# Kernel tuning notes

Hardware: AMD Instinct MI355X
Metric: run time of the kernel (lower is better)

Reference implementation:

```python
import jax, jax.numpy as jnp
import numpy as np

N_NODES = 50000
N_EDGES = 600000
IN_DIM = 128
LATENT = 128
OUT_DIM = 40
NUM_LAYERS = 2


def setup_inputs() -> dict:
    key = jax.random.key(0)
    ks = jax.random.split(key, 8)
    nodes_feats = jax.random.normal(ks[0], (N_NODES, IN_DIM), dtype=jnp.float32)
    adj_list = jax.random.randint(ks[1], (N_EDGES, 2), 0, N_NODES, dtype=jnp.int64)
    s_in = 1.0 / np.sqrt(IN_DIM)
    s_cb = 1.0 / np.sqrt(2 * LATENT)
    s_out = 1.0 / np.sqrt(LATENT)
    W_in = jax.random.uniform(ks[2], (IN_DIM, LATENT), jnp.float32, -s_in, s_in)
    b_in = jnp.zeros((LATENT,), jnp.float32)
    W_comb = jax.random.uniform(ks[3], (NUM_LAYERS, 2 * LATENT, LATENT), jnp.float32, -s_cb, s_cb)
    b_comb = jnp.zeros((NUM_LAYERS, LATENT), jnp.float32)
    W_out = jax.random.uniform(ks[4], (LATENT, OUT_DIM), jnp.float32, -s_out, s_out)
    b_out = jnp.zeros((OUT_DIM,), jnp.float32)
    return {"nodes_feats": nodes_feats, "adj_list": adj_list, "W_in": W_in, "b_in": b_in,
            "W_comb": W_comb, "b_comb": b_comb, "W_out": W_out, "b_out": b_out}


def reference(nodes_feats, adj_list, W_in, b_in, W_comb, b_comb, W_out, b_out):
    n = nodes_feats.shape[0]
    fro = adj_list[:, 0]
    to = adj_list[:, 1]
    # initialize: project input features to latent space
    h = jax.nn.relu(nodes_feats @ W_in + b_in)  # [N, LATENT]
    # in-degree for mean aggregation (replaces per-node Python stack+mean)
    deg = jax.ops.segment_sum(jnp.ones(fro.shape[0], h.dtype), to, num_segments=n)
    inv_deg = 1.0 / jnp.maximum(deg, 1.0)  # guard isolated nodes
    for l in range(W_comb.shape[0]):
        # gather neighbor feats along edges, scatter-add to destinations, mean
        msg = jax.ops.segment_sum(h[fro], to, num_segments=n) * inv_deg[:, None]
        # combine: ReLU(Linear([node || message]))
        h = jax.nn.relu(jnp.concatenate([h, msg], axis=-1) @ W_comb[l] + b_comb[l])
    # output head (logits for CrossEntropyLoss)
    return h @ W_out + b_out
```

## Files before the change

kernel.cpp:

```cpp
#include <hip/hip_runtime.h>
#include <hip/hip_fp16.h>

#define N_NODES 50000
#define N_EDGES 600000
#define NBLK 49

typedef unsigned int u32;
typedef _Float16 v8h __attribute__((ext_vector_type(8)));
typedef _Float16 v4h __attribute__((ext_vector_type(4)));
typedef float v4f __attribute__((ext_vector_type(4)));

__device__ __forceinline__ float2 h2f2(u32 u) {
    __half2 h = *(__half2*)&u;
    return __half22float2(h);
}

__device__ __forceinline__ int calc_mode(const int* __restrict__ adj_w) {
    int l = threadIdx.x & 63;
    unsigned long long b = __ballot(adj_w[2 * l + 1] != 0);
    return (b == 0ull) ? 1 : 0;
}
__device__ __forceinline__ int adj_to(const int* a, int m, int e) {
    return m ? a[4 * e + 2] : a[2 * e + 1];
}
__device__ __forceinline__ int adj_fro(const int* a, int m, int e) {
    return m ? a[4 * e] : a[2 * e];
}

#define COUNT_B 2344
#define WPREP_B 344
#define IN_B    1563

__global__ void k_count_prep(const int* __restrict__ adj_w, int* __restrict__ deg,
                             const float* __restrict__ W_in,
                             const float* __restrict__ W_comb,
                             const float* __restrict__ W_out,
                             _Float16* __restrict__ WinT,
                             _Float16* __restrict__ WcombT,
                             _Float16* __restrict__ WoutT) {
    if (blockIdx.x < COUNT_B) {
        int m = calc_mode(adj_w);
        int e = blockIdx.x * 256 + threadIdx.x;
        if (e < N_EDGES) atomicAdd(&deg[adj_to(adj_w, m, e)], 1);
        return;
    }
    int idx = (blockIdx.x - COUNT_B) * 256 + threadIdx.x;
    if (idx < 16384) {
        int n = idx & 127, k = idx >> 7;
        WinT[n * 128 + k] = (_Float16)W_in[k * 128 + n];
    } else if (idx < 16384 + 65536) {
        int j = idx - 16384;
        int l = j >> 15, r = j & 32767;
        int n = r & 127, k = r >> 7;
        WcombT[l * 32768 + n * 256 + k] = (_Float16)W_comb[l * 32768 + k * 128 + n];
    } else if (idx < 16384 + 65536 + 6144) {
        int j = idx - 81920;
        int n = j >> 7, k = j & 127;
        WoutT[n * 128 + k] = (n < 40) ? (_Float16)W_out[k * 40 + n] : (_Float16)0.f;
    }
}

__global__ void k_scan1(const int* __restrict__ deg, int* __restrict__ row_ptr,
                        int* __restrict__ bsum) {
    __shared__ int s[1024];
    int tid = threadIdx.x, i = blockIdx.x * 1024 + tid;
    int v = (i < N_NODES) ? deg[i] : 0;
    s[tid] = v;
    __syncthreads();
    for (int off = 1; off < 1024; off <<= 1) {
        int t = (tid >= off) ? s[tid - off] : 0;
        __syncthreads();
        s[tid] += t;
        __syncthreads();
    }
    if (i < N_NODES) row_ptr[i] = s[tid] - v;
    if (tid == 1023) bsum[blockIdx.x] = s[1023];
}

__global__ void k_scan23(const int* __restrict__ deg, int* __restrict__ row_ptr,
                         const int* __restrict__ bsum, int* __restrict__ cursor,
                         float* __restrict__ inv_deg) {
    __shared__ int sbase;
    int tid = threadIdx.x;
    if (tid < 64) {
        int v = (tid < NBLK && tid < (int)blockIdx.x) ? bsum[tid] : 0;
#pragma unroll
        for (int off = 32; off > 0; off >>= 1) v += __shfl_down(v, off);
        if (tid == 0) sbase = v;
    }
    __syncthreads();
    int i = blockIdx.x * 1024 + tid;
    if (i < N_NODES) {
        int rp = row_ptr[i] + sbase;
        row_ptr[i] = rp;
        cursor[i] = rp;
        inv_deg[i] = 1.0f / fmaxf((float)deg[i], 1.0f);
    }
    if (i == 0) row_ptr[N_NODES] = N_EDGES;
}

__global__ __launch_bounds__(256, 2) void k_fill_in(const int* __restrict__ adj_w,
                                                    int* __restrict__ cursor,
                                                    int* __restrict__ edge_src,
                                                    const float* __restrict__ X,
                                                    const _Float16* __restrict__ WT,
                                                    const float* __restrict__ bias,
                                                    _Float16* __restrict__ h) {
    __shared__ __align__(16) _Float16 xs[32][136];
    if (blockIdx.x < COUNT_B) {
        int m = calc_mode(adj_w);
        int e = blockIdx.x * 256 + threadIdx.x;
        if (e < N_EDGES) {
            int to = adj_to(adj_w, m, e);
            int slot = atomicAdd(&cursor[to], 1);
            edge_src[slot] = adj_fro(adj_w, m, e);
        }
        return;
    }
    const int t0 = threadIdx.x, w = t0 >> 6, l = t0 & 63;
    const int R0 = (blockIdx.x - COUNT_B) * 32;
    const float4* X4 = (const float4*)X;
#pragma unroll
    for (int i = 0; i < 4; i++) {
        int idx = i * 256 + t0;
        int row = idx >> 5, c4 = idx & 31;
        int rr = R0 + row;
        if (rr > N_NODES - 1) rr = N_NODES - 1;
        float4 v = X4[(size_t)rr * 32 + c4];
        v4h hv = {(_Float16)v.x, (_Float16)v.y, (_Float16)v.z, (_Float16)v.w};
        *(v4h*)&xs[row][c4 * 4] = hv;
    }
    const int ch = w & 1, rh = w >> 1;
    v8h wf[4][4];
#pragma unroll
    for (int t = 0; t < 4; t++)
#pragma unroll
        for (int s = 0; s < 4; s++) {
            int n = ch * 64 + t * 16 + (l & 15);
            int k = s * 32 + (l >> 4) * 8;
            wf[t][s] = *(const v8h*)&WT[n * 128 + k];
        }
    v4f acc[4];
#pragma unroll
    for (int t = 0; t < 4; t++) acc[t] = (v4f){0.f, 0.f, 0.f, 0.f};
    __syncthreads();
#pragma unroll
    for (int s = 0; s < 4; s++) {
        v8h a = *(const v8h*)&xs[rh * 16 + (l & 15)][s * 32 + (l >> 4) * 8];
#pragma unroll
        for (int t = 0; t < 4; t++)
            acc[t] = __builtin_amdgcn_mfma_f32_16x16x32_f16(a, wf[t][s], acc[t], 0, 0, 0);
    }
#pragma unroll
    for (int t = 0; t < 4; t++) {
        int col = ch * 64 + t * 16 + (l & 15);
        float b = bias[col];
#pragma unroll
        for (int i = 0; i < 4; i++) {
            int row = R0 + rh * 16 + (l >> 4) * 4 + i;
            if (row < N_NODES)
                h[(size_t)row * 128 + col] = (_Float16)fmaxf(acc[t][i] + b, 0.f);
        }
    }
}

__global__ __launch_bounds__(256) void k_gather(const uint2* __restrict__ h4,
                                                uint2* __restrict__ msg4,
                                                const int* __restrict__ row_ptr,
                                                const int* __restrict__ edge_src,
                                                const float* __restrict__ inv_deg) {
    const int w = threadIdx.x >> 6, l = threadIdx.x & 63;
    const int half = l >> 5, c = l & 31;
    const int wid = blockIdx.x * 4 + w, nw = gridDim.x * 4;
    for (int row = wid; row < N_NODES; row += nw) {
        const int e0 = row_ptr[row], e1 = row_ptr[row + 1];
        float a0 = 0.f, a1 = 0.f, a2 = 0.f, a3 = 0.f;
        for (int bse = e0; bse < e1; bse += 8) {
            uint2 v[4];
#pragma unroll
            for (int i = 0; i < 4; i++) {
                int ee = bse + 2 * i + half;
                int idx = (ee < e1) ? ee : (e1 - 1);
                v[i] = h4[(size_t)edge_src[idx] * 32 + c];
            }
#pragma unroll
            for (int i = 0; i < 4; i++) {
                if (bse + 2 * i + half < e1) {
                    float2 f0 = h2f2(v[i].x), f1 = h2f2(v[i].y);
                    a0 += f0.x;
                    a1 += f0.y;
                    a2 += f1.x;
                    a3 += f1.y;
                }
            }
        }
        a0 += __shfl_xor(a0, 32);
        a1 += __shfl_xor(a1, 32);
        a2 += __shfl_xor(a2, 32);
        a3 += __shfl_xor(a3, 32);
        if (half == 0) {
            const float inv = inv_deg[row];
            __half2 o0 = __floats2half2_rn(a0 * inv, a1 * inv);
            __half2 o1 = __floats2half2_rn(a2 * inv, a3 * inv);
            uint2 o;
            o.x = *(u32*)&o0;
            o.y = *(u32*)&o1;
            msg4[(size_t)row * 32 + c] = o;
        }
    }
}

__global__ __launch_bounds__(256, 2) void k_layer(const _Float16* __restrict__ hin,
                                                  const _Float16* __restrict__ msg,
                                                  const _Float16* __restrict__ WT,
                                                  const float* __restrict__ bias,
                                                  _Float16* __restrict__ hout) {
    __shared__ __align__(16) _Float16 xs[64][264];
    const int t0 = threadIdx.x, w = t0 >> 6, l = t0 & 63;
    const int R0 = blockIdx.x * 64;
    const uint4* h4 = (const uint4*)hin;
    const uint4* m4 = (const uint4*)msg;
#pragma unroll
    for (int i = 0; i < 8; i++) {
        int idx = i * 256 + t0;
        int row = idx >> 5, c16 = idx & 31;
        int rr = R0 + row;
        if (rr > N_NODES - 1) rr = N_NODES - 1;
        uint4 v = (c16 < 16) ? h4[(size_t)rr * 16 + c16] : m4[(size_t)rr * 16 + (c16 - 16)];
        *(uint4*)&xs[row][c16 * 8] = v;
    }
    const int ch = w & 1, rh = w >> 1;
    v8h wf[4][8];
#pragma unroll
    for (int t = 0; t < 4; t++)
#pragma unroll
        for (int s = 0; s < 8; s++) {
            int n = ch * 64 + t * 16 + (l & 15);
            int k = s * 32 + (l >> 4) * 8;
            wf[t][s] = *(const v8h*)&WT[n * 256 + k];
        }
    v4f acc[2][4];
#pragma unroll
    for (int sub = 0; sub < 2; sub++)
#pragma unroll
        for (int t = 0; t < 4; t++) acc[sub][t] = (v4f){0.f, 0.f, 0.f, 0.f};
    __syncthreads();
#pragma unroll
    for (int s = 0; s < 8; s++) {
#pragma unroll
        for (int sub = 0; sub < 2; sub++) {
            v8h a = *(const v8h*)&xs[rh * 32 + sub * 16 + (l & 15)][s * 32 + (l >> 4) * 8];
#pragma unroll
            for (int t = 0; t < 4; t++)
                acc[sub][t] = __builtin_amdgcn_mfma_f32_16x16x32_f16(a, wf[t][s], acc[sub][t], 0, 0, 0);
        }
    }
#pragma unroll
    for (int sub = 0; sub < 2; sub++)
#pragma unroll
        for (int t = 0; t < 4; t++) {
            int col = ch * 64 + t * 16 + (l & 15);
            float b = bias[col];
#pragma unroll
            for (int i = 0; i < 4; i++) {
                int row = R0 + rh * 32 + sub * 16 + (l >> 4) * 4 + i;
                if (row < N_NODES)
                    hout[(size_t)row * 128 + col] = (_Float16)fmaxf(acc[sub][t][i] + b, 0.f);
            }
        }
}

__global__ __launch_bounds__(256, 2) void k_layer_out(const _Float16* __restrict__ hin,
                                                      const _Float16* __restrict__ msg,
                                                      const _Float16* __restrict__ WT,
                                                      const float* __restrict__ bias,
                                                      const _Float16* __restrict__ WoT,
                                                      const float* __restrict__ bias_o,
                                                      float* __restrict__ outp) {
    __shared__ __align__(16) _Float16 xs[64][264];
    const int t0 = threadIdx.x, w = t0 >> 6, l = t0 & 63;
    const int R0 = blockIdx.x * 64;
    const uint4* h4 = (const uint4*)hin;
    const uint4* m4 = (const uint4*)msg;
#pragma unroll
    for (int i = 0; i < 8; i++) {
        int idx = i * 256 + t0;
        int row = idx >> 5, c16 = idx & 31;
        int rr = R0 + row;
        if (rr > N_NODES - 1) rr = N_NODES - 1;
        uint4 v = (c16 < 16) ? h4[(size_t)rr * 16 + c16] : m4[(size_t)rr * 16 + (c16 - 16)];
        *(uint4*)&xs[row][c16 * 8] = v;
    }
    const int ch = w & 1, rh = w >> 1;
    v8h wf[4][8];
#pragma unroll
    for (int t = 0; t < 4; t++)
#pragma unroll
        for (int s = 0; s < 8; s++) {
            int n = ch * 64 + t * 16 + (l & 15);
            int k = s * 32 + (l >> 4) * 8;
            wf[t][s] = *(const v8h*)&WT[n * 256 + k];
        }
    v4f acc[2][4];
#pragma unroll
    for (int sub = 0; sub < 2; sub++)
#pragma unroll
        for (int t = 0; t < 4; t++) acc[sub][t] = (v4f){0.f, 0.f, 0.f, 0.f};
    __syncthreads();
#pragma unroll
    for (int s = 0; s < 8; s++) {
#pragma unroll
        for (int sub = 0; sub < 2; sub++) {
            v8h a = *(const v8h*)&xs[rh * 32 + sub * 16 + (l & 15)][s * 32 + (l >> 4) * 8];
#pragma unroll
            for (int t = 0; t < 4; t++)
                acc[sub][t] = __builtin_amdgcn_mfma_f32_16x16x32_f16(a, wf[t][s], acc[sub][t], 0, 0, 0);
        }
    }
    __syncthreads();
    _Float16* hs = &xs[0][0];
#pragma unroll
    for (int sub = 0; sub < 2; sub++)
#pragma unroll
        for (int t = 0; t < 4; t++) {
            int col = ch * 64 + t * 16 + (l & 15);
            float b = bias[col];
#pragma unroll
            for (int i = 0; i < 4; i++) {
                int lrow = rh * 32 + sub * 16 + (l >> 4) * 4 + i;
                hs[lrow * 136 + col] = (_Float16)fmaxf(acc[sub][t][i] + b, 0.f);
            }
        }
    v8h wo[3][4];
#pragma unroll
    for (int t = 0; t < 3; t++)
#pragma unroll
        for (int s = 0; s < 4; s++) {
            int n = t * 16 + (l & 15);
            int k = s * 32 + (l >> 4) * 8;
            wo[t][s] = *(const v8h*)&WoT[n * 128 + k];
        }
    v4f acc2[3];
#pragma unroll
    for (int t = 0; t < 3; t++) acc2[t] = (v4f){0.f, 0.f, 0.f, 0.f};
    __syncthreads();
#pragma unroll
    for (int s = 0; s < 4; s++) {
        v8h a = *(const v8h*)&hs[(w * 16 + (l & 15)) * 136 + s * 32 + (l >> 4) * 8];
#pragma unroll
        for (int t = 0; t < 3; t++)
            acc2[t] = __builtin_amdgcn_mfma_f32_16x16x32_f16(a, wo[t][s], acc2[t], 0, 0, 0);
    }
#pragma unroll
    for (int t = 0; t < 3; t++) {
        int col = t * 16 + (l & 15);
        if (col < 40) {
            float b = bias_o[col];
#pragma unroll
            for (int i = 0; i < 4; i++) {
                int row = R0 + w * 16 + (l >> 4) * 4 + i;
                if (row < N_NODES) outp[(size_t)row * 40 + col] = acc2[t][i] + b;
            }
        }
    }
}

extern "C" void kernel_launch(void* const* d_in, const int* in_sizes, int n_in,
                              void* d_out, int out_size, void* d_ws, size_t ws_size,
                              hipStream_t stream) {
    int ix[8] = {0, 1, 2, 3, 4, 5, 6, 7};
    int tmp[8] = {-1, -1, -1, -1, -1, -1, -1, -1};
    for (int i = 0; i < n_in && i < 8; i++) {
        switch (in_sizes[i]) {
            case 6400000: tmp[0] = i; break;
            case 1200000: case 2400000: tmp[1] = i; break;
            case 16384:   tmp[2] = i; break;
            case 128:     tmp[3] = i; break;
            case 65536:   tmp[4] = i; break;
            case 256:     tmp[5] = i; break;
            case 5120:    tmp[6] = i; break;
            case 40:      tmp[7] = i; break;
        }
    }
    int found = 0;
    for (int j = 0; j < 8; j++) found += (tmp[j] >= 0);
    if (found == 8) for (int j = 0; j < 8; j++) ix[j] = tmp[j];

    const float* X      = (const float*)d_in[ix[0]];
    const int*   adj_w  = (const int*)d_in[ix[1]];
    const float* W_in   = (const float*)d_in[ix[2]];
    const float* b_in   = (const float*)d_in[ix[3]];
    const float* W_comb = (const float*)d_in[ix[4]];
    const float* b_comb = (const float*)d_in[ix[5]];
    const float* W_out  = (const float*)d_in[ix[6]];
    const float* b_out  = (const float*)d_in[ix[7]];
    float* out = (float*)d_out;

    char* base = (char*)d_ws;
    int*      deg      = (int*)(base + 0);
    int*      row_ptr  = (int*)(base + 200000);
    int*      cursor   = (int*)(base + 400004);
    float*    inv_deg  = (float*)(base + 600004);
    int*      edge_src = (int*)(base + 800008);
    _Float16* WinT     = (_Float16*)(base + 3200016);
    _Float16* WcombT   = (_Float16*)(base + 3232784);
    _Float16* WoutT    = (_Float16*)(base + 3363856);
    _Float16* hA       = (_Float16*)(base + 3376144);
    _Float16* hB       = (_Float16*)(base + 16176144);
    _Float16* msg      = (_Float16*)(base + 28976144);
    int*      bsum     = (int*)hA;

    hipMemsetAsync(deg, 0, N_NODES * sizeof(int), stream);
    k_count_prep<<<COUNT_B + WPREP_B, 256, 0, stream>>>(adj_w, deg, W_in, W_comb, W_out,
                                                        WinT, WcombT, WoutT);
    k_scan1<<<NBLK, 1024, 0, stream>>>(deg, row_ptr, bsum);
    k_scan23<<<NBLK, 1024, 0, stream>>>(deg, row_ptr, bsum, cursor, inv_deg);
    k_fill_in<<<COUNT_B + IN_B, 256, 0, stream>>>(adj_w, cursor, edge_src, X, WinT, b_in, hA);

    k_gather<<<2048, 256, 0, stream>>>((const uint2*)hA, (uint2*)msg, row_ptr, edge_src, inv_deg);
    k_layer<<<782, 256, 0, stream>>>(hA, msg, WcombT, b_comb, hB);

    k_gather<<<2048, 256, 0, stream>>>((const uint2*)hB, (uint2*)msg, row_ptr, edge_src, inv_deg);
    k_layer_out<<<782, 256, 0, stream>>>(hB, msg, WcombT + 32768, b_comb + 128,
                                         WoutT, b_out, out);
}
```

Before: 273.3 us.

## Record per-edge atomic rank during counting to drop second atomic pass in CSR fill

The degree-count pass now stores each edge's return value from atomicAdd as a rank. The fill pass then places edges at row_ptr[to]+rank with plain stores, so the second round of atomics on a cursor array goes away. Each thread also handles 8 edges with batched loads and atomics instead of one. The cost is an extra 2.4 MB rank array that is written and read back, plus fewer blocks in the count and fill grids.

```diff
diff --git a/kernel.cpp b/kernel.cpp
--- a/kernel.cpp
+++ b/kernel.cpp
@@ -27,24 +27,38 @@
     return m ? a[4 * e] : a[2 * e];
 }
 
-#define COUNT_B 2344
+#define CNT_B   293
 #define WPREP_B 344
 #define IN_B    1563
 
 __global__ void k_count_prep(const int* __restrict__ adj_w, int* __restrict__ deg,
+                             int* __restrict__ rank,
                              const float* __restrict__ W_in,
                              const float* __restrict__ W_comb,
                              const float* __restrict__ W_out,
                              _Float16* __restrict__ WinT,
                              _Float16* __restrict__ WcombT,
                              _Float16* __restrict__ WoutT) {
-    if (blockIdx.x < COUNT_B) {
+    if (blockIdx.x < CNT_B) {
         int m = calc_mode(adj_w);
-        int e = blockIdx.x * 256 + threadIdx.x;
-        if (e < N_EDGES) atomicAdd(&deg[adj_to(adj_w, m, e)], 1);
+        int base = blockIdx.x * 2048 + threadIdx.x;
+        int to[8], r[8];
+#pragma unroll
+        for (int i = 0; i < 8; i++) {
+            int e = base + i * 256;
+            to[i] = (e < N_EDGES) ? adj_to(adj_w, m, e) : -1;
+        }
+#pragma unroll
+        for (int i = 0; i < 8; i++)
+            if (to[i] >= 0) r[i] = atomicAdd(&deg[to[i]], 1);
+#pragma unroll
+        for (int i = 0; i < 8; i++) {
+            int e = base + i * 256;
+            if (e < N_EDGES) rank[e] = r[i];
+        }
         return;
     }
-    int idx = (blockIdx.x - COUNT_B) * 256 + threadIdx.x;
+    int idx = (blockIdx.x - CNT_B) * 256 + threadIdx.x;
     if (idx < 16384) {
         int n = idx & 127, k = idx >> 7;
         WinT[n * 128 + k] = (_Float16)W_in[k * 128 + n];
@@ -78,8 +92,7 @@
 }
 
 __global__ void k_scan23(const int* __restrict__ deg, int* __restrict__ row_ptr,
-                         const int* __restrict__ bsum, int* __restrict__ cursor,
-                         float* __restrict__ inv_deg) {
+                         const int* __restrict__ bsum, float* __restrict__ inv_deg) {
     __shared__ int sbase;
     int tid = threadIdx.x;
     if (tid < 64) {
@@ -91,34 +104,43 @@
     __syncthreads();
     int i = blockIdx.x * 1024 + tid;
     if (i < N_NODES) {
-        int rp = row_ptr[i] + sbase;
-        row_ptr[i] = rp;
-        cursor[i] = rp;
+        row_ptr[i] = row_ptr[i] + sbase;
         inv_deg[i] = 1.0f / fmaxf((float)deg[i], 1.0f);
     }
     if (i == 0) row_ptr[N_NODES] = N_EDGES;
 }
 
 __global__ __launch_bounds__(256, 2) void k_fill_in(const int* __restrict__ adj_w,
-                                                    int* __restrict__ cursor,
+                                                    const int* __restrict__ row_ptr,
+                                                    const int* __restrict__ rank,
                                                     int* __restrict__ edge_src,
                                                     const float* __restrict__ X,
                                                     const _Float16* __restrict__ WT,
                                                     const float* __restrict__ bias,
                                                     _Float16* __restrict__ h) {
     __shared__ __align__(16) _Float16 xs[32][136];
-    if (blockIdx.x < COUNT_B) {
+    if (blockIdx.x < CNT_B) {
         int m = calc_mode(adj_w);
-        int e = blockIdx.x * 256 + threadIdx.x;
-        if (e < N_EDGES) {
-            int to = adj_to(adj_w, m, e);
-            int slot = atomicAdd(&cursor[to], 1);
-            edge_src[slot] = adj_fro(adj_w, m, e);
-        }
+        int base = blockIdx.x * 2048 + threadIdx.x;
+        int to[8], fro[8], rk[8];
+#pragma unroll
+        for (int i = 0; i < 8; i++) {
+            int e = base + i * 256;
+            if (e < N_EDGES) {
+                to[i] = adj_to(adj_w, m, e);
+                fro[i] = adj_fro(adj_w, m, e);
+                rk[i] = rank[e];
+            } else {
+                to[i] = -1;
+            }
+        }
+#pragma unroll
+        for (int i = 0; i < 8; i++)
+            if (to[i] >= 0) edge_src[row_ptr[to[i]] + rk[i]] = fro[i];
         return;
     }
     const int t0 = threadIdx.x, w = t0 >> 6, l = t0 & 63;
-    const int R0 = (blockIdx.x - COUNT_B) * 32;
+    const int R0 = (blockIdx.x - CNT_B) * 32;
     const float4* X4 = (const float4*)X;
 #pragma unroll
     for (int i = 0; i < 4; i++) {
@@ -399,23 +421,24 @@
     char* base = (char*)d_ws;
     int*      deg      = (int*)(base + 0);
     int*      row_ptr  = (int*)(base + 200000);
-    int*      cursor   = (int*)(base + 400004);
-    float*    inv_deg  = (float*)(base + 600004);
-    int*      edge_src = (int*)(base + 800008);
-    _Float16* WinT     = (_Float16*)(base + 3200016);
-    _Float16* WcombT   = (_Float16*)(base + 3232784);
-    _Float16* WoutT    = (_Float16*)(base + 3363856);
-    _Float16* hA       = (_Float16*)(base + 3376144);
-    _Float16* hB       = (_Float16*)(base + 16176144);
-    _Float16* msg      = (_Float16*)(base + 28976144);
+    int*      rank     = (int*)(base + 400004);
+    float*    inv_deg  = (float*)(base + 2800004);
+    int*      edge_src = (int*)(base + 3000008);
+    _Float16* WinT     = (_Float16*)(base + 5400016);
+    _Float16* WcombT   = (_Float16*)(base + 5432784);
+    _Float16* WoutT    = (_Float16*)(base + 5563856);
+    _Float16* hA       = (_Float16*)(base + 5576144);
+    _Float16* hB       = (_Float16*)(base + 18376144);
+    _Float16* msg      = (_Float16*)(base + 31176144);
     int*      bsum     = (int*)hA;
 
     hipMemsetAsync(deg, 0, N_NODES * sizeof(int), stream);
-    k_count_prep<<<COUNT_B + WPREP_B, 256, 0, stream>>>(adj_w, deg, W_in, W_comb, W_out,
-                                                        WinT, WcombT, WoutT);
+    k_count_prep<<<CNT_B + WPREP_B, 256, 0, stream>>>(adj_w, deg, rank, W_in, W_comb, W_out,
+                                                      WinT, WcombT, WoutT);
     k_scan1<<<NBLK, 1024, 0, stream>>>(deg, row_ptr, bsum);
-    k_scan23<<<NBLK, 1024, 0, stream>>>(deg, row_ptr, bsum, cursor, inv_deg);
-    k_fill_in<<<COUNT_B + IN_B, 256, 0, stream>>>(adj_w, cursor, edge_src, X, WinT, b_in, hA);
+    k_scan23<<<NBLK, 1024, 0, stream>>>(deg, row_ptr, bsum, inv_deg);
+    k_fill_in<<<CNT_B + IN_B, 256, 0, stream>>>(adj_w, row_ptr, rank, edge_src,
+                                                X, WinT, b_in, hA);
 
     k_gather<<<2048, 256, 0, stream>>>((const uint2*)hA, (uint2*)msg, row_ptr, edge_src, inv_deg);
     k_layer<<<782, 256, 0, stream>>>(hA, msg, WcombT, b_comb, hB);
```

Result: faster. 254.8 us (-6.7%).
